# Performance work log

Hardware: AMD Instinct MI355X
Metric: run time of the kernel (lower is better)

Reference implementation:

```python
import jax, jax.numpy as jnp
import numpy as np

B = 16384
TEXT_D = 768
TECH_D = 256
IN_D = TEXT_D + TECH_D  # 1024
OUT_D = 1024
E = 8


def setup_inputs() -> dict:
    key = jax.random.key(0)
    ks = jax.random.split(key, 8)
    s_in = 1.0 / np.sqrt(IN_D)
    s_out = 1.0 / np.sqrt(OUT_D)
    return {
        "text_features": jax.random.normal(ks[0], (B, TEXT_D), jnp.float32),
        "technical_features": jax.random.normal(ks[1], (B, TECH_D), jnp.float32),
        # stacked expert params: layer1 [E, IN_D, OUT_D], layer2 [E, OUT_D, OUT_D]
        "W1": jax.random.uniform(ks[2], (E, IN_D, OUT_D), jnp.float32, -s_in, s_in),
        "b1": jax.random.uniform(ks[3], (E, OUT_D), jnp.float32, -s_in, s_in),
        "W2": jax.random.uniform(ks[4], (E, OUT_D, OUT_D), jnp.float32, -s_out, s_out),
        "b2": jax.random.uniform(ks[5], (E, OUT_D), jnp.float32, -s_out, s_out),
        # gating network
        "Wg": jax.random.uniform(ks[6], (IN_D, E), jnp.float32, -s_in, s_in),
        "bg": jax.random.uniform(ks[7], (E,), jnp.float32, -s_in, s_in),
    }


def reference(text_features, technical_features, W1, b1, W2, b2, Wg, bg):
    x = jnp.concatenate([text_features, technical_features], axis=-1)  # [B, IN_D]
    gates = jax.nn.softmax(x @ Wg + bg, axis=-1)                       # [B, E]
    h = jax.nn.relu(jnp.einsum('bi,eio->beo', x, W1) + b1[None])       # [B, E, OUT_D]
    y = jnp.einsum('beo,eop->bep', h, W2) + b2[None]                   # [B, E, OUT_D]
    return jnp.einsum('be,bep->bp', gates, y)                          # [B, OUT_D]
```

## Files before the change

### kernel.cpp

```cpp
#include <hip/hip_runtime.h>
#include <hip/hip_bf16.h>

#define NB 16384
#define TEXT_D 768
#define TECH_D 256
#define IND 1024
#define OUTD 1024
#define NE 8
#define KH2 4096

typedef unsigned short u16;
typedef __bf16 bf16x8 __attribute__((ext_vector_type(8)));
typedef float f32x4 __attribute__((ext_vector_type(4)));

__device__ __forceinline__ u16 f2bf(float f) {
  union { float f; unsigned int u; } x; x.f = f;
  unsigned int u = x.u;
  return (u16)((u + 0x7FFFu + ((u >> 16) & 1u)) >> 16);
}

__device__ __forceinline__ void gload_lds16(const void* g, void* l) {
  __builtin_amdgcn_global_load_lds(
      (const __attribute__((address_space(1))) unsigned int*)g,
      (__attribute__((address_space(3))) unsigned int*)l, 16, 0, 0);
}

__global__ __launch_bounds__(256) void convert_gates(
    const float* __restrict__ text, const float* __restrict__ tech,
    const float* __restrict__ Wg, const float* __restrict__ bg,
    u16* __restrict__ xb, float* __restrict__ gates) {
  int t = threadIdx.x;
  int wave = t >> 6, lane = t & 63;
  int row = blockIdx.x * 4 + wave;

  float acc[NE];
#pragma unroll
  for (int e = 0; e < NE; ++e) acc[e] = 0.f;

#pragma unroll
  for (int j = 0; j < 4; ++j) {
    int col = j * 256 + lane * 4;
    float4 v = (j < 3) ? *(const float4*)&text[(size_t)row * TEXT_D + col]
                       : *(const float4*)&tech[(size_t)row * TECH_D + lane * 4];
    ushort4 o = make_ushort4(f2bf(v.x), f2bf(v.y), f2bf(v.z), f2bf(v.w));
    *(ushort4*)&xb[(size_t)row * IND + col] = o;
    const float* wp = &Wg[(size_t)col * NE];
    float xv[4] = {v.x, v.y, v.z, v.w};
#pragma unroll
    for (int i = 0; i < 4; ++i) {
      float4 w0 = *(const float4*)&wp[i * NE];
      float4 w1 = *(const float4*)&wp[i * NE + 4];
      acc[0] = fmaf(xv[i], w0.x, acc[0]);
      acc[1] = fmaf(xv[i], w0.y, acc[1]);
      acc[2] = fmaf(xv[i], w0.z, acc[2]);
      acc[3] = fmaf(xv[i], w0.w, acc[3]);
      acc[4] = fmaf(xv[i], w1.x, acc[4]);
      acc[5] = fmaf(xv[i], w1.y, acc[5]);
      acc[6] = fmaf(xv[i], w1.z, acc[6]);
      acc[7] = fmaf(xv[i], w1.w, acc[7]);
    }
  }
#pragma unroll
  for (int off = 32; off; off >>= 1)
#pragma unroll
    for (int e = 0; e < NE; ++e) acc[e] += __shfl_xor(acc[e], off);

#pragma unroll
  for (int e = 0; e < NE; ++e) acc[e] += bg[e];
  float mx = acc[0];
#pragma unroll
  for (int e = 1; e < NE; ++e) mx = fmaxf(mx, acc[e]);
  float s = 0.f;
#pragma unroll
  for (int e = 0; e < NE; ++e) { acc[e] = expf(acc[e] - mx); s += acc[e]; }
  float inv = 1.f / s;
  if (lane < NE) gates[(size_t)row * NE + lane] = acc[lane] * inv;
}

__global__ __launch_bounds__(256) void transpose_w12(
    const float* __restrict__ W1, const float* __restrict__ W2,
    u16* __restrict__ W1t, u16* __restrict__ W2t) {
  __shared__ u16 tile[64][65];
  int bid = blockIdx.x;
  int half = bid >> 11;
  int b2 = bid & 2047;
  int e = b2 >> 8;
  int tb = b2 & 255;
  int r0 = (tb >> 4) * 64;
  int c0 = (tb & 15) * 64;
  const float* We; u16* Wte; int ostride;
  if (half == 0) {
    We = W1 + (size_t)e * IND * OUTD;
    Wte = W1t + ((size_t)e << 20);
    ostride = 1024;
  } else {
    We = W2 + (size_t)e * IND * OUTD;
    Wte = W2t + ((size_t)(e >> 2) << 22) + (size_t)(e & 3) * 1024;
    ostride = KH2;
  }
  int t = threadIdx.x;
  int tr = t >> 4;
  int s  = t & 15;
  int tc = s * 4;
#pragma unroll
  for (int j = 0; j < 4; ++j) {
    int row = j * 16 + tr;
    float4 v = *(const float4*)&We[(size_t)(r0 + row) * OUTD + c0 + tc];
    tile[row][tc + 0] = f2bf(v.x);
    tile[row][tc + 1] = f2bf(v.y);
    tile[row][tc + 2] = f2bf(v.z);
    tile[row][tc + 3] = f2bf(v.w);
  }
  __syncthreads();
#pragma unroll
  for (int j = 0; j < 4; ++j) {
    int row = j * 16 + tr;
    ushort4 o;
    if (half == 0) {
      o = make_ushort4(tile[tc + 0][row], tile[tc + 1][row],
                       tile[tc + 2][row], tile[tc + 3][row]);
    } else {
      o = make_ushort4(tile[s][row], tile[s + 16][row],
                       tile[s + 32][row], tile[s + 48][row]);
    }
    *(ushort4*)&Wte[(size_t)(c0 + row) * ostride + r0 + tc] = o;
  }
}

#define BAR() asm volatile("s_barrier" ::: "memory")
#define VM0() asm volatile("s_waitcnt vmcnt(0)" ::: "memory")
#define VM4() asm volatile("s_waitcnt vmcnt(4)" ::: "memory")
#define VM8() asm volatile("s_waitcnt vmcnt(8)" ::: "memory")

template <int SLOT, int K>
__device__ __forceinline__ void stage_slot(
    const u16* __restrict__ pA, const u16* __restrict__ pB, char* sb, int k0,
    int ch0, int rsub, int koff, int lbyte) {
#pragma unroll
  for (int j = 0; j < 2; ++j) {
    int ch = ch0 + j;
    int r;
    if constexpr (SLOT == 0)      r = (ch >> 3) * 128 + (ch & 7) * 8 + rsub;
    else if constexpr (SLOT == 3) r = 64 + (ch >> 3) * 128 + (ch & 7) * 8 + rsub;
    else if constexpr (SLOT == 1) r = (ch >> 2) * 64 + (ch & 3) * 8 + rsub;
    else                          r = (ch >> 2) * 64 + 32 + (ch & 3) * 8 + rsub;
    const u16* g = (SLOT == 0 || SLOT == 3) ? pA : pB;
    char* lb = sb + ((SLOT == 0 || SLOT == 3) ? 0 : 32768) + r * 128 + lbyte;
    gload_lds16(g + (size_t)r * K + k0 + koff, lb);
  }
}

template <int QH>
__device__ __forceinline__ void load_a(const char* rb, int wr, int lr, int hi,
                                       int swr, bf16x8 (&a)[4][2]) {
#pragma unroll
  for (int i = 0; i < 4; ++i)
#pragma unroll
    for (int ks = 0; ks < 2; ++ks)
      a[i][ks] = *(const bf16x8*)(rb + (wr * 128 + QH * 64 + i * 16 + lr) * 128
                                  + ((ks * 64 + hi * 16) ^ swr));
}

template <int NH>
__device__ __forceinline__ void load_b(const char* rb, int wc, int lr, int hi,
                                       int swr, bf16x8 (&b)[2][2]) {
#pragma unroll
  for (int q = 0; q < 2; ++q)
#pragma unroll
    for (int ks = 0; ks < 2; ++ks)
      b[q][ks] = *(const bf16x8*)(rb + 32768 +
                                  (wc * 64 + (NH * 2 + q) * 16 + lr) * 128
                                  + ((ks * 64 + hi * 16) ^ swr));
}

template <int MH, int NH>
__device__ __forceinline__ void mfma_quad(const bf16x8 (&a)[4][2],
                                          const bf16x8 (&b)[2][2],
                                          f32x4 (&acc)[8][4]) {
  __builtin_amdgcn_s_setprio(1);
#pragma unroll
  for (int i = 0; i < 4; ++i)
#pragma unroll
    for (int q = 0; q < 2; ++q) {
      acc[MH*4+i][NH*2+q] = __builtin_amdgcn_mfma_f32_16x16x32_bf16(
          a[i][0], b[q][0], acc[MH*4+i][NH*2+q], 0, 0, 0);
      acc[MH*4+i][NH*2+q] = __builtin_amdgcn_mfma_f32_16x16x32_bf16(
          a[i][1], b[q][1], acc[MH*4+i][NH*2+q], 0, 0, 0);
    }
  __builtin_amdgcn_s_setprio(0);
}

template <int RB, int K, int MODE>
__device__ __forceinline__ void ktile(
    const u16* __restrict__ pA, const u16* __restrict__ pB, char* lds,
    int kH1, int kH0, int ch0, int rsub, int koff, int lbyte,
    int wr, int wc, int lr, int hi, int swr,
    bf16x8 (&a)[4][2], bf16x8 (&b0)[2][2], bf16x8 (&b1)[2][2],
    f32x4 (&acc)[8][4]) {
  const char* rb = lds + RB * 65536;
  char* nbuf = lds + (RB ^ 1) * 65536;
  char* tbuf = lds + RB * 65536;
  load_a<0>(rb, wr, lr, hi, swr, a);
  load_b<0>(rb, wc, lr, hi, swr, b0);
  if constexpr (MODE < 2) {
    stage_slot<2, K>(pA, pB, nbuf, kH1, ch0, rsub, koff, lbyte);
    stage_slot<3, K>(pA, pB, nbuf, kH1, ch0, rsub, koff, lbyte);
  }
  BAR();
  mfma_quad<0, 0>(a, b0, acc);
  if constexpr (MODE == 2) { VM0(); } else { VM8(); }
  BAR();
  load_b<1>(rb, wc, lr, hi, swr, b1);
  BAR();
  mfma_quad<0, 1>(a, b1, acc);
  BAR();
  load_a<1>(rb, wr, lr, hi, swr, a);
  BAR();
  mfma_quad<1, 0>(a, b0, acc);
  BAR();
  if constexpr (MODE == 0) {
    stage_slot<0, K>(pA, pB, tbuf, kH0, ch0, rsub, koff, lbyte);
    stage_slot<1, K>(pA, pB, tbuf, kH0, ch0, rsub, koff, lbyte);
  }
  BAR();
  mfma_quad<1, 1>(a, b1, acc);
  if constexpr (MODE == 0) { VM8(); }
  else if constexpr (MODE == 1) { VM4(); }
  BAR();
}

template <int K>
__device__ __forceinline__ void core256(const u16* __restrict__ pA,
                                        const u16* __restrict__ pB,
                                        char* lds, int t, f32x4 (&acc)[8][4]) {
  constexpr int KT = K / 64;
  static_assert(KT >= 4 && (KT & 1) == 0, "KT must be even >= 4");
  const int l = t & 63;
  const int w = t >> 6;
  const int wr = w >> 2, wc = w & 3;
  const int lr = l & 15, hi = l >> 4;
  const int rsub = l >> 3;
  const int koff = ((l & 7) ^ rsub) << 3;
  const int lbyte = (l & 7) * 16;
  const int ch0 = w * 2;
  const int swr = (lr & 7) << 4;

  bf16x8 a[4][2], b0[2][2], b1[2][2];

  stage_slot<0, K>(pA, pB, lds, 0, ch0, rsub, koff, lbyte);
  stage_slot<1, K>(pA, pB, lds, 0, ch0, rsub, koff, lbyte);
  stage_slot<2, K>(pA, pB, lds, 0, ch0, rsub, koff, lbyte);
  stage_slot<3, K>(pA, pB, lds, 0, ch0, rsub, koff, lbyte);
  stage_slot<0, K>(pA, pB, lds + 65536, 64, ch0, rsub, koff, lbyte);
  stage_slot<1, K>(pA, pB, lds + 65536, 64, ch0, rsub, koff, lbyte);
  VM8(); BAR();

  for (int T = 0; T < KT - 2; T += 2) {
    ktile<0, K, 0>(pA, pB, lds, (T + 1) * 64, (T + 2) * 64, ch0, rsub, koff,
                   lbyte, wr, wc, lr, hi, swr, a, b0, b1, acc);
    ktile<1, K, 0>(pA, pB, lds, (T + 2) * 64, (T + 3) * 64, ch0, rsub, koff,
                   lbyte, wr, wc, lr, hi, swr, a, b0, b1, acc);
  }
  ktile<0, K, 1>(pA, pB, lds, (KT - 1) * 64, 0, ch0, rsub, koff,
                 lbyte, wr, wc, lr, hi, swr, a, b0, b1, acc);
  ktile<1, K, 2>(pA, pB, lds, 0, 0, ch0, rsub, koff,
                 lbyte, wr, wc, lr, hi, swr, a, b0, b1, acc);
  VM0();
}

__global__ __launch_bounds__(512, 2) void gemm1(
    const u16* __restrict__ xb, const u16* __restrict__ W1t,
    const float* __restrict__ b1, const float* __restrict__ gates,
    u16* __restrict__ Hg, int eg0) {
  __shared__ char lds[131072];
  int t = threadIdx.x;
  int nwg = gridDim.x, cpx = nwg >> 3, bid = blockIdx.x;
  int swz = (bid & 7) * cpx + (bid >> 3);
  int nb = swz & 3, ee = (swz >> 2) & 3, mb = swz >> 4;
  int e = eg0 + ee;

  f32x4 acc[8][4] = {};
  core256<1024>(xb + (size_t)mb * 256 * 1024,
                W1t + ((size_t)e << 20) + (size_t)nb * 256 * 1024,
                lds, t, acc);

  int l = t & 63, w = t >> 6, wr = w >> 2, wc = w & 3, lr = l & 15, hi = l >> 4;
  int m0 = mb * 256 + wr * 128 + hi * 4;
  int n0 = nb * 256 + wc * 64 + lr;
  int nst = nb * 256 + wc * 64 + lr * 4;
  const float* b1e = b1 + e * OUTD;
  float bv[4];
#pragma unroll
  for (int nn = 0; nn < 4; ++nn) bv[nn] = b1e[n0 + nn * 16];
#pragma unroll
  for (int m = 0; m < 8; ++m) {
#pragma unroll
    for (int r = 0; r < 4; ++r) {
      int row = m0 + m * 16 + r;
      float g = gates[(size_t)row * NE + e];
      ushort4 o;
      o.x = f2bf(g * fmaxf(acc[m][0][r] + bv[0], 0.f));
      o.y = f2bf(g * fmaxf(acc[m][1][r] + bv[1], 0.f));
      o.z = f2bf(g * fmaxf(acc[m][2][r] + bv[2], 0.f));
      o.w = f2bf(g * fmaxf(acc[m][3][r] + bv[3], 0.f));
      *(ushort4*)&Hg[(size_t)row * KH2 + ee * 1024 + nst] = o;
    }
  }
}

template <bool FIRST>
__global__ __launch_bounds__(512, 2) void gemm2(
    const u16* __restrict__ Hg, const u16* __restrict__ W2th,
    const float* __restrict__ b2h, const float* __restrict__ gates,
    float* __restrict__ out, int eg0) {
  __shared__ char lds[131072];
  int t = threadIdx.x;
  int nwg = gridDim.x, cpx = nwg >> 3, bid = blockIdx.x;
  int swz = (bid & 7) * cpx + (bid >> 3);
  int nb = swz & 3, mb = swz >> 2;

  f32x4 acc[8][4] = {};
  core256<KH2>(Hg + (size_t)mb * 256 * KH2, W2th + (size_t)nb * 256 * KH2,
               lds, t, acc);

  int l = t & 63, w = t >> 6, wr = w >> 2, wc = w & 3, lr = l & 15, hi = l >> 4;
  int m0 = mb * 256 + wr * 128 + hi * 4;
  int n0 = nb * 256 + wc * 64 + lr;

  float bcol[4][4];
#pragma unroll
  for (int nn = 0; nn < 4; ++nn)
#pragma unroll
    for (int j = 0; j < 4; ++j)
      bcol[nn][j] = b2h[j * OUTD + n0 + nn * 16];

#pragma unroll
  for (int m = 0; m < 8; ++m) {
#pragma unroll
    for (int r = 0; r < 4; ++r) {
      int row = m0 + m * 16 + r;
      float4 ga = *(const float4*)&gates[(size_t)row * NE + eg0];
#pragma unroll
      for (int nn = 0; nn < 4; ++nn) {
        float bias = ga.x * bcol[nn][0] + ga.y * bcol[nn][1] +
                     ga.z * bcol[nn][2] + ga.w * bcol[nn][3];
        size_t oi = (size_t)row * OUTD + n0 + nn * 16;
        float v = acc[m][nn][r] + bias;
        if (FIRST) out[oi] = v;
        else       out[oi] += v;
      }
    }
  }
}

extern "C" void kernel_launch(void* const* d_in, const int* in_sizes, int n_in,
                              void* d_out, int out_size, void* d_ws, size_t ws_size,
                              hipStream_t stream) {
  (void)in_sizes; (void)n_in; (void)out_size; (void)ws_size;
  const float* text = (const float*)d_in[0];
  const float* tech = (const float*)d_in[1];
  const float* W1   = (const float*)d_in[2];
  const float* b1   = (const float*)d_in[3];
  const float* W2   = (const float*)d_in[4];
  const float* b2   = (const float*)d_in[5];
  const float* Wg   = (const float*)d_in[6];
  const float* bg   = (const float*)d_in[7];
  float* out = (float*)d_out;

  char* p = (char*)d_ws;
  u16* xb  = (u16*)p;  p += (size_t)NB * IND * 2;
  u16* W1t = (u16*)p;  p += (size_t)NE * IND * OUTD * 2;
  u16* W2t = (u16*)p;  p += (size_t)NE * OUTD * OUTD * 2;
  float* gates = (float*)p; p += (size_t)NB * NE * 4;
  u16* Hg  = (u16*)p;

  convert_gates<<<dim3(NB / 4), dim3(256), 0, stream>>>(text, tech, Wg, bg, xb, gates);
  transpose_w12<<<dim3(4096), dim3(256), 0, stream>>>(W1, W2, W1t, W2t);

  for (int h = 0; h < 2; ++h) {
    int eg0 = h * 4;
    gemm1<<<dim3(1024), dim3(512), 0, stream>>>(xb, W1t, b1, gates, Hg, eg0);
    const u16* W2th = W2t + ((size_t)h << 22);
    const float* b2h = b2 + (size_t)eg0 * OUTD;
    if (h == 0)
      gemm2<true><<<dim3(256), dim3(512), 0, stream>>>(Hg, W2th, b2h, gates, out, eg0);
    else
      gemm2<false><<<dim3(256), dim3(512), 0, stream>>>(Hg, W2th, b2h, gates, out, eg0);
  }
}
```

Baseline: 591.7 us.

## Restructure GEMM k-loop into simple double-buffered pipeline with fewer barriers

Replaces the interleaved half-tile staging scheme with a plain ping-pong double buffer: separate A and B LDS regions, the whole next k-tile staged while computing the current one, and two barriers per tile instead of about seven. The setprio calls are hoisted around pairs of MFMA groups, and the vmcnt waits change to match the new issue order. The aim is to cut barrier and scheduling overhead in the inner loop. In exchange, global loads are issued less finely interleaved with compute, which may expose more memory latency, and correctness depends on the new vmcnt counts and swizzled addressing staying consistent.

```diff
diff --git a/kernel.cpp b/kernel.cpp
--- a/kernel.cpp
+++ b/kernel.cpp
@@ -129,12 +129,12 @@
 
 #define BAR() asm volatile("s_barrier" ::: "memory")
 #define VM0() asm volatile("s_waitcnt vmcnt(0)" ::: "memory")
-#define VM4() asm volatile("s_waitcnt vmcnt(4)" ::: "memory")
-#define VM8() asm volatile("s_waitcnt vmcnt(8)" ::: "memory")
+#define VM2() asm volatile("s_waitcnt vmcnt(2)" ::: "memory")
+#define VM6() asm volatile("s_waitcnt vmcnt(6)" ::: "memory")
 
 template <int SLOT, int K>
 __device__ __forceinline__ void stage_slot(
-    const u16* __restrict__ pA, const u16* __restrict__ pB, char* sb, int k0,
+    const u16* __restrict__ g, char* buf, int k0,
     int ch0, int rsub, int koff, int lbyte) {
 #pragma unroll
   for (int j = 0; j < 2; ++j) {
@@ -144,9 +144,7 @@
     else if constexpr (SLOT == 3) r = 64 + (ch >> 3) * 128 + (ch & 7) * 8 + rsub;
     else if constexpr (SLOT == 1) r = (ch >> 2) * 64 + (ch & 3) * 8 + rsub;
     else                          r = (ch >> 2) * 64 + 32 + (ch & 3) * 8 + rsub;
-    const u16* g = (SLOT == 0 || SLOT == 3) ? pA : pB;
-    char* lb = sb + ((SLOT == 0 || SLOT == 3) ? 0 : 32768) + r * 128 + lbyte;
-    gload_lds16(g + (size_t)r * K + k0 + koff, lb);
+    gload_lds16(g + (size_t)r * K + k0 + koff, buf + r * 128 + lbyte);
   }
 }
 
@@ -168,7 +166,7 @@
   for (int q = 0; q < 2; ++q)
 #pragma unroll
     for (int ks = 0; ks < 2; ++ks)
-      b[q][ks] = *(const bf16x8*)(rb + 32768 +
+      b[q][ks] = *(const bf16x8*)(rb +
                                   (wc * 64 + (NH * 2 + q) * 16 + lr) * 128
                                   + ((ks * 64 + hi * 16) ^ swr));
 }
@@ -177,7 +175,6 @@
 __device__ __forceinline__ void mfma_quad(const bf16x8 (&a)[4][2],
                                           const bf16x8 (&b)[2][2],
                                           f32x4 (&acc)[8][4]) {
-  __builtin_amdgcn_s_setprio(1);
 #pragma unroll
   for (int i = 0; i < 4; ++i)
 #pragma unroll
@@ -187,46 +184,38 @@
       acc[MH*4+i][NH*2+q] = __builtin_amdgcn_mfma_f32_16x16x32_bf16(
           a[i][1], b[q][1], acc[MH*4+i][NH*2+q], 0, 0, 0);
     }
-  __builtin_amdgcn_s_setprio(0);
-}
-
-template <int RB, int K, int MODE>
-__device__ __forceinline__ void ktile(
-    const u16* __restrict__ pA, const u16* __restrict__ pB, char* lds,
-    int kH1, int kH0, int ch0, int rsub, int koff, int lbyte,
+}
+
+template <bool LAST, int K>
+__device__ __forceinline__ void tile_body(
+    const u16* __restrict__ pA, const u16* __restrict__ pB,
+    const char* rA, const char* rB, char* sA, char* sB, int kN,
+    int ch0, int rsub, int koff, int lbyte,
     int wr, int wc, int lr, int hi, int swr,
     bf16x8 (&a)[4][2], bf16x8 (&b0)[2][2], bf16x8 (&b1)[2][2],
     f32x4 (&acc)[8][4]) {
-  const char* rb = lds + RB * 65536;
-  char* nbuf = lds + (RB ^ 1) * 65536;
-  char* tbuf = lds + RB * 65536;
-  load_a<0>(rb, wr, lr, hi, swr, a);
-  load_b<0>(rb, wc, lr, hi, swr, b0);
-  if constexpr (MODE < 2) {
-    stage_slot<2, K>(pA, pB, nbuf, kH1, ch0, rsub, koff, lbyte);
-    stage_slot<3, K>(pA, pB, nbuf, kH1, ch0, rsub, koff, lbyte);
-  }
+  if constexpr (!LAST) {
+    stage_slot<0, K>(pA, sA, kN, ch0, rsub, koff, lbyte);
+    stage_slot<1, K>(pB, sB, kN, ch0, rsub, koff, lbyte);
+    stage_slot<2, K>(pB, sB, kN, ch0, rsub, koff, lbyte);
+  }
+  load_a<0>(rA, wr, lr, hi, swr, a);
+  load_b<0>(rB, wc, lr, hi, swr, b0);
+  load_b<1>(rB, wc, lr, hi, swr, b1);
+  __builtin_amdgcn_s_setprio(1);
+  mfma_quad<0, 0>(a, b0, acc);
+  mfma_quad<0, 1>(a, b1, acc);
+  __builtin_amdgcn_s_setprio(0);
+  if constexpr (!LAST) { VM6(); } else { VM0(); }
   BAR();
-  mfma_quad<0, 0>(a, b0, acc);
-  if constexpr (MODE == 2) { VM0(); } else { VM8(); }
-  BAR();
-  load_b<1>(rb, wc, lr, hi, swr, b1);
-  BAR();
-  mfma_quad<0, 1>(a, b1, acc);
-  BAR();
-  load_a<1>(rb, wr, lr, hi, swr, a);
-  BAR();
+  if constexpr (!LAST)
+    stage_slot<3, K>(pA, sA, kN, ch0, rsub, koff, lbyte);
+  load_a<1>(rA, wr, lr, hi, swr, a);
+  __builtin_amdgcn_s_setprio(1);
   mfma_quad<1, 0>(a, b0, acc);
-  BAR();
-  if constexpr (MODE == 0) {
-    stage_slot<0, K>(pA, pB, tbuf, kH0, ch0, rsub, koff, lbyte);
-    stage_slot<1, K>(pA, pB, tbuf, kH0, ch0, rsub, koff, lbyte);
-  }
-  BAR();
   mfma_quad<1, 1>(a, b1, acc);
-  if constexpr (MODE == 0) { VM8(); }
-  else if constexpr (MODE == 1) { VM4(); }
-  BAR();
+  __builtin_amdgcn_s_setprio(0);
+  if constexpr (!LAST) { VM2(); BAR(); }
 }
 
 template <int K>
@@ -234,7 +223,7 @@
                                         const u16* __restrict__ pB,
                                         char* lds, int t, f32x4 (&acc)[8][4]) {
   constexpr int KT = K / 64;
-  static_assert(KT >= 4 && (KT & 1) == 0, "KT must be even >= 4");
+  static_assert(KT >= 2, "KT must be >= 2");
   const int l = t & 63;
   const int w = t >> 6;
   const int wr = w >> 2, wc = w & 3;
@@ -245,27 +234,30 @@
   const int ch0 = w * 2;
   const int swr = (lr & 7) << 4;
 
+  char* A0 = lds;
+  char* A1 = lds + 32768;
+  char* B0 = lds + 65536;
+  char* B1 = lds + 98304;
+
   bf16x8 a[4][2], b0[2][2], b1[2][2];
 
-  stage_slot<0, K>(pA, pB, lds, 0, ch0, rsub, koff, lbyte);
-  stage_slot<1, K>(pA, pB, lds, 0, ch0, rsub, koff, lbyte);
-  stage_slot<2, K>(pA, pB, lds, 0, ch0, rsub, koff, lbyte);
-  stage_slot<3, K>(pA, pB, lds, 0, ch0, rsub, koff, lbyte);
-  stage_slot<0, K>(pA, pB, lds + 65536, 64, ch0, rsub, koff, lbyte);
-  stage_slot<1, K>(pA, pB, lds + 65536, 64, ch0, rsub, koff, lbyte);
-  VM8(); BAR();
-
-  for (int T = 0; T < KT - 2; T += 2) {
-    ktile<0, K, 0>(pA, pB, lds, (T + 1) * 64, (T + 2) * 64, ch0, rsub, koff,
-                   lbyte, wr, wc, lr, hi, swr, a, b0, b1, acc);
-    ktile<1, K, 0>(pA, pB, lds, (T + 2) * 64, (T + 3) * 64, ch0, rsub, koff,
-                   lbyte, wr, wc, lr, hi, swr, a, b0, b1, acc);
-  }
-  ktile<0, K, 1>(pA, pB, lds, (KT - 1) * 64, 0, ch0, rsub, koff,
-                 lbyte, wr, wc, lr, hi, swr, a, b0, b1, acc);
-  ktile<1, K, 2>(pA, pB, lds, 0, 0, ch0, rsub, koff,
-                 lbyte, wr, wc, lr, hi, swr, a, b0, b1, acc);
-  VM0();
+  stage_slot<0, K>(pA, A0, 0, ch0, rsub, koff, lbyte);
+  stage_slot<1, K>(pB, B0, 0, ch0, rsub, koff, lbyte);
+  stage_slot<2, K>(pB, B0, 0, ch0, rsub, koff, lbyte);
+  stage_slot<3, K>(pA, A0, 0, ch0, rsub, koff, lbyte);
+  VM0(); BAR();
+
+  char *rA = A0, *rB = B0, *sA = A1, *sB = B1;
+  for (int T = 0; T < KT - 1; ++T) {
+    tile_body<false, K>(pA, pB, rA, rB, sA, sB, (T + 1) * 64,
+                        ch0, rsub, koff, lbyte, wr, wc, lr, hi, swr,
+                        a, b0, b1, acc);
+    char* x = rA; rA = sA; sA = x;
+    x = rB; rB = sB; sB = x;
+  }
+  tile_body<true, K>(pA, pB, rA, rB, sA, sB, 0,
+                     ch0, rsub, koff, lbyte, wr, wc, lr, hi, swr,
+                     a, b0, b1, acc);
 }
 
 __global__ __launch_bounds__(512, 2) void gemm1(
```

After: 581.1 us. No clear change (-1.8%).
